# Performance work log

Measured on AMD Instinct MI355X. Metric: run time of the kernel, lower is better.

The kernel has to match this reference:

```python
import jax, jax.numpy as jnp
import numpy as np
import math

N_HEADS = 8
INPUT_DIM = 128
EMBED_DIM = 128
KEY_DIM = EMBED_DIM // N_HEADS  # 16, val_dim == key_dim
BATCH = 4
GRAPH = 2048


def setup_inputs() -> dict:
    key = jax.random.key(0)
    k1, k2, k3, k4, k5 = jax.random.split(key, 5)
    h = jax.random.normal(k1, (BATCH, GRAPH, INPUT_DIM), dtype=jnp.float32)
    # torch.rand -> uniform [0,1)
    W_query = jax.random.uniform(k2, (N_HEADS, INPUT_DIM, KEY_DIM), dtype=jnp.float32)
    W_key = jax.random.uniform(k3, (N_HEADS, INPUT_DIM, KEY_DIM), dtype=jnp.float32)
    W_val = jax.random.uniform(k4, (N_HEADS, INPUT_DIM, KEY_DIM), dtype=jnp.float32)
    W_out = jax.random.uniform(k5, (N_HEADS, KEY_DIM, EMBED_DIM), dtype=jnp.float32)
    return {"h": h, "W_query": W_query, "W_key": W_key, "W_val": W_val, "W_out": W_out}


def reference(h, W_query, W_key, W_val, W_out):
    # q defaults to h (self-attention)
    norm = 1.0 / math.sqrt(KEY_DIM)
    # per-head projections: [H, B, N, dk]
    Q = jnp.einsum('bnd,hdk->hbnk', h, W_query)
    K = jnp.einsum('bnd,hdk->hbnk', h, W_key)
    V = jnp.einsum('bnd,hdv->hbnv', h, W_val)
    compat = norm * jnp.einsum('hbqk,hbnk->hbqn', Q, K)  # [H, B, Nq, N]
    attn = jax.nn.softmax(compat, axis=-1)
    heads = jnp.einsum('hbqn,hbnv->hbqv', attn, V)  # [H, B, Nq, dv]
    out = jnp.einsum('hbqv,hve->bqe', heads, W_out)  # [B, Nq, E]
    return out
```

## Files before the change

### kernel.cpp

```cpp
#include <hip/hip_runtime.h>

typedef __attribute__((ext_vector_type(4))) float f32x4;
typedef __attribute__((ext_vector_type(8))) short bf16x8;

constexpr int NH = 8, D = 128, DK = 16, B = 4, N = 2048;
constexpr int KTILE = 128;
constexpr int NTILES = N / KTILE;
constexpr int TILE_SHORTS = 6144;
constexpr float QSCALE = 0.36067376022224085f;

__device__ __forceinline__ unsigned short f2bf(float f) {
    union { float f; unsigned u; } v; v.f = f;
    return (unsigned short)((v.u + 0x7fffu + ((v.u >> 16) & 1u)) >> 16);
}
__device__ __forceinline__ float bf2f(unsigned short h) {
    union { unsigned u; float f; } v; v.u = ((unsigned)h) << 16; return v.f;
}
__device__ __forceinline__ unsigned pack2(float a, float b) {
    union { float f; unsigned u; } x, y; x.f = a; y.f = b;
    return (x.u >> 16) | (y.u & 0xFFFF0000u);
}
__device__ __forceinline__ float fexp2(float x) {
    float r; asm("v_exp_f32 %0, %1" : "=v"(r) : "v"(x)); return r;
}
__device__ __forceinline__ float fmax3(float a, float b, float c) {
    float r; asm("v_max3_f32 %0, %1, %2, %3" : "=v"(r) : "v"(a), "v"(b), "v"(c));
    return r;
}

__global__ __launch_bounds__(256) void wprep_kernel(
    const float* __restrict__ Wq, const float* __restrict__ Wk,
    const float* __restrict__ Wv, const float* __restrict__ Wo,
    unsigned short* __restrict__ Wf, unsigned short* __restrict__ Wof)
{
    const int t = blockIdx.x * 256 + threadIdx.x;
    if (t < 49152) {
        const int p = t >> 14, r = t & 16383;
        const int head = r >> 11, d = (r >> 4) & 127, kk = r & 15;
        const float wv = (p == 0 ? Wq : p == 1 ? Wk : Wv)[r];
        const unsigned short hi = f2bf(wv);
        const unsigned short lo = f2bf(wv - bf2f(hi));
        const int c = p * 8 + head, s = d >> 4, dd = d & 15;
        const int ch = dd >> 3, j = dd & 7;
        Wf[((c * 8 + s) * 64 + kk + 16 * ch) * 8 + j] = hi;
        Wf[((c * 8 + s) * 64 + kk + 16 * (2 + ch)) * 8 + j] = lo;
    } else {
        const int r = t - 49152;
        const int head = r >> 11, v = (r >> 7) & 15, e = r & 127;
        const float wv = Wo[r];
        const unsigned short hi = f2bf(wv);
        const unsigned short lo = f2bf(wv - bf2f(hi));
        const int c = e >> 4, s = head, ch = v >> 3, j = v & 7;
        Wof[((c * 8 + s) * 64 + (e & 15) + 16 * ch) * 8 + j] = hi;
        Wof[((c * 8 + s) * 64 + (e & 15) + 16 * (2 + ch)) * 8 + j] = lo;
    }
}

constexpr int GR = 32;
__global__ __launch_bounds__(256) void qkv_gemm(
    const float* __restrict__ h, const unsigned short* __restrict__ Wf,
    float* __restrict__ Q, unsigned short* __restrict__ KV)
{
    const int cg6 = blockIdx.x % 6;
    const int cg = cg6 >> 1;
    const int hg = cg6 & 1;
    const int row0 = (blockIdx.x / 6) * GR;
    const int b = row0 >> 11, n0 = row0 & (N - 1);
    const int t = threadIdx.x, w = t >> 6, l = t & 63;
    __shared__ unsigned short hf[8][2][64][8];
    __shared__ unsigned short wfl[4][8][64][8];

    {
        const unsigned short* wsrc = Wf + ((size_t)cg * 8 + hg * 4) * 4096;
        unsigned short* wdst = (unsigned short*)wfl;
        #pragma unroll
        for (int i = 0; i < 8; ++i) {
            const int idx = (t + i * 256) * 8;
            *(uint4*)&wdst[idx] = *(const uint4*)&wsrc[idx];
        }
    }
    #pragma unroll
    for (int pass = 0; pass < 4; ++pass) {
        const int rb = pass * 8 + (t >> 5);
        const int d0 = (t & 31) * 4;
        float4 hv = *(const float4*)&h[(size_t)(row0 + rb) * D + d0];
        const int s = d0 >> 4, ch = (d0 & 15) >> 3, j0 = d0 & 7;
        ushort4 hiv, lov;
        unsigned short* hp = (unsigned short*)&hiv;
        unsigned short* lp = (unsigned short*)&lov;
        #pragma unroll
        for (int i = 0; i < 4; ++i) {
            const float x = ((const float*)&hv)[i];
            const unsigned short hi = f2bf(x);
            hp[i] = hi;
            lp[i] = f2bf(x - bf2f(hi));
        }
        *(ushort4*)&hf[s][rb >> 4][(rb & 15) + 16 * ch][j0] = hiv;
        *(ushort4*)&hf[s][rb >> 4][(rb & 15) + 16 * (2 + ch)][j0] = lov;
    }
    __syncthreads();

    f32x4 acc[2];
    #pragma unroll
    for (int i = 0; i < 2; ++i) acc[i] = (f32x4){0.f, 0.f, 0.f, 0.f};

    for (int s = 0; s < 8; ++s) {
        bf16x8 b1 = *(const bf16x8*)&hf[s][w & 1][l][0];
        bf16x8 b2 = *(const bf16x8*)&hf[s][w & 1][l ^ 32][0];
        #pragma unroll
        for (int ct = 0; ct < 2; ++ct) {
            const int c4 = (w >> 1) * 2 + ct;
            bf16x8 af = *(const bf16x8*)&wfl[c4][s][l][0];
            acc[ct] = __builtin_amdgcn_mfma_f32_16x16x32_bf16(af, b1, acc[ct], 0, 0, 0);
            acc[ct] = __builtin_amdgcn_mfma_f32_16x16x32_bf16(af, b2, acc[ct], 0, 0, 0);
        }
    }

    const int n = n0 + (w & 1) * 16 + (l & 15);
    const int rl = n & 127;
    const int kk0 = (l >> 4) * 4;
    #pragma unroll
    for (int ct = 0; ct < 2; ++ct) {
        const int head = hg * 4 + (w >> 1) * 2 + ct;
        const int hb = head * B + b;
        if (cg == 0) {
            float4 o;
            o.x = acc[ct][0]; o.y = acc[ct][1]; o.z = acc[ct][2]; o.w = acc[ct][3];
            *(float4*)&Q[((size_t)hb * N + n) * DK + kk0] = o;
        } else {
            unsigned short* tb = KV + (size_t)hb * NTILES * TILE_SHORTS
                               + (size_t)(n >> 7) * TILE_SHORTS;
            if (cg == 1) {
                const int gs = kk0 >> 3, j0 = kk0 & 7;
                const int kb2 = rl >> 5, kap = rl & 31;
                const int sub = 2 * kb2 + ((kap >> 2) & 1);
                const int row16 = 4 * (kap >> 3) + (kap & 3);
                ushort4 sh, sl;
                unsigned short* shp = (unsigned short*)&sh;
                unsigned short* slp = (unsigned short*)&sl;
                #pragma unroll
                for (int r = 0; r < 4; ++r) {
                    const unsigned short hi = f2bf(acc[ct][r]);
                    shp[r] = hi;
                    slp[r] = f2bf(acc[ct][r] - bf2f(hi));
                }
                *(ushort4*)&tb[sub * 512 + (row16 + 16 * gs) * 8 + j0] = sh;
                *(ushort4*)&tb[sub * 512 + (row16 + 16 * (2 + gs)) * 8 + j0] = sl;
            } else {
                #pragma unroll
                for (int r = 0; r < 4; ++r) {
                    const int kk = kk0 + r;
                    tb[4096 + kk * 128 + ((rl >> 3) ^ (kk & 7)) * 8 + (rl & 7)]
                        = f2bf(acc[ct][r]);
                }
            }
        }
    }
}

__global__ __launch_bounds__(512, 4) void attn_kernel(
    const float* __restrict__ Q, const unsigned short* __restrict__ KV,
    float* __restrict__ Hd)
{
    const int bid = blockIdx.x;
    const int inner = bid >> 3;
    const int hb = (bid & 7) * 4 + (inner >> 4);
    const int qt = inner & 15;
    const int t = threadIdx.x, w = t >> 6, l = t & 63;
    const int q16 = l & 15, g = l >> 4;
    const size_t qbase = (size_t)hb * N * DK;
    const char* kvb = (const char*)(KV + (size_t)hb * NTILES * TILE_SHORTS);

    __shared__ unsigned short smem[2][TILE_SHORTS];

    const int qrow = qt * 128 + w * 16 + q16;
    bf16x8 qhi, qlo;
    {
        const float* qp = Q + qbase + (size_t)qrow * DK + (g & 1) * 8;
        float4 qa = *(const float4*)qp, qb = *(const float4*)(qp + 4);
        #pragma unroll
        for (int i = 0; i < 8; ++i) {
            const float x = (i < 4 ? ((const float*)&qa)[i] : ((const float*)&qb)[i - 4]) * QSCALE;
            const unsigned short hi = f2bf(x);
            qhi[i] = (short)hi;
            qlo[i] = (short)f2bf(x - bf2f(hi));
        }
    }
    const bf16x8 qf1 = (g < 2) ? qhi : qlo;
    const bf16x8 qf2 = (g < 2) ? qlo : qhi;

    union { unsigned u[4]; bf16x8 v; } ones;
    #pragma unroll
    for (int i = 0; i < 4; ++i) ones.u[i] = 0x3F803F80u;

    f32x4 oacc = {0.f, 0.f, 0.f, 0.f};
    f32x4 lacc = {0.f, 0.f, 0.f, 0.f};
    float m = 0.0f;

    uint4 s0 = *(const uint4*)(kvb + t * 16);
    uint4 s1;
    if (t < 256) s1 = *(const uint4*)(kvb + 8192 + t * 16);
    *(uint4*)((char*)&smem[0][0] + t * 16) = s0;
    if (t < 256) *(uint4*)((char*)&smem[0][0] + 8192 + t * 16) = s1;

    int cur = 0;
    for (int tile = 0; tile < NTILES; ++tile) {
        __syncthreads();
        if (tile + 1 < NTILES) {
            const char* gt = kvb + (size_t)(tile + 1) * 12288;
            s0 = *(const uint4*)(gt + t * 16);
            if (t < 256) s1 = *(const uint4*)(gt + 8192 + t * 16);
        }
        const char* buf = (const char*)&smem[cur][0];

        f32x4 aA[4], aB[4];
        const f32x4 minit = {-m, -m, -m, -m};
        __builtin_amdgcn_s_setprio(1);
        #pragma unroll
        for (int kb = 0; kb < 4; ++kb) {
            bf16x8 kA = *(const bf16x8*)(buf + (2 * kb) * 1024 + l * 16);
            bf16x8 kB = *(const bf16x8*)(buf + (2 * kb + 1) * 1024 + l * 16);
            aA[kb] = __builtin_amdgcn_mfma_f32_16x16x32_bf16(kA, qf1, minit, 0, 0, 0);
            aA[kb] = __builtin_amdgcn_mfma_f32_16x16x32_bf16(kA, qf2, aA[kb], 0, 0, 0);
            aB[kb] = __builtin_amdgcn_mfma_f32_16x16x32_bf16(kB, qf1, minit, 0, 0, 0);
            aB[kb] = __builtin_amdgcn_mfma_f32_16x16x32_bf16(kB, qf2, aB[kb], 0, 0, 0);
        }
        __builtin_amdgcn_s_setprio(0);

        float tm = -3.0e38f;
        #pragma unroll
        for (int kb = 0; kb < 4; ++kb) {
            tm = fmax3(fmax3(aA[kb][0], aA[kb][1], aA[kb][2]),
                       fmax3(aA[kb][3], aB[kb][0], aB[kb][1]),
                       fmax3(aB[kb][2], aB[kb][3], tm));
        }
        if (tile == 0 || !__all(tm <= -30.0f)) {
            if (tile == 0) {
                float d = fmaxf(tm, __shfl_xor(tm, 16));
                d = fmaxf(d, __shfl_xor(d, 32));
                m = d;
                #pragma unroll
                for (int kb = 0; kb < 4; ++kb) {
                    #pragma unroll
                    for (int i = 0; i < 4; ++i) { aA[kb][i] -= d; aB[kb][i] -= d; }
                }
            } else if (!__all(tm <= 8.0f)) {
                float d = fmaxf(tm, __shfl_xor(tm, 16));
                d = fmaxf(d, __shfl_xor(d, 32));
                const float dd = fmaxf(d, 0.f);
                const float sc = fexp2(-dd);
                m += dd;
                oacc *= sc;
                lacc *= sc;
                #pragma unroll
                for (int kb = 0; kb < 4; ++kb) {
                    #pragma unroll
                    for (int i = 0; i < 4; ++i) { aA[kb][i] -= dd; aB[kb][i] -= dd; }
                }
            }
            #pragma unroll
            for (int kb = 0; kb < 4; ++kb) {
                #pragma unroll
                for (int i = 0; i < 4; ++i) {
                    aA[kb][i] = fexp2(aA[kb][i]);
                    aB[kb][i] = fexp2(aB[kb][i]);
                }
            }
            __builtin_amdgcn_s_setprio(1);
            #pragma unroll
            for (int kb = 0; kb < 4; ++kb) {
                union { unsigned u[4]; bf16x8 v; } pf;
                pf.u[0] = pack2(aA[kb][0], aA[kb][1]);
                pf.u[1] = pack2(aA[kb][2], aA[kb][3]);
                pf.u[2] = pack2(aB[kb][0], aB[kb][1]);
                pf.u[3] = pack2(aB[kb][2], aB[kb][3]);
                bf16x8 vf = *(const bf16x8*)(buf + 8192 + q16 * 256 + (((kb * 4 + g) ^ (q16 & 7)) * 16));
                oacc = __builtin_amdgcn_mfma_f32_16x16x32_bf16(vf, pf.v, oacc, 0, 0, 0);
                lacc = __builtin_amdgcn_mfma_f32_16x16x32_bf16(ones.v, pf.v, lacc, 0, 0, 0);
            }
            __builtin_amdgcn_s_setprio(0);
        }

        if (tile + 1 < NTILES) {
            char* nb = (char*)&smem[cur ^ 1][0];
            *(uint4*)(nb + t * 16) = s0;
            if (t < 256) *(uint4*)(nb + 8192 + t * 16) = s1;
        }
        cur ^= 1;
    }

    const float invl = 1.f / lacc[0];
    float4 o;
    o.x = oacc[0] * invl; o.y = oacc[1] * invl;
    o.z = oacc[2] * invl; o.w = oacc[3] * invl;
    *(float4*)(Hd + qbase + (size_t)qrow * DK + g * 4) = o;
}

constexpr int OGR = 16;
__global__ __launch_bounds__(256) void out_gemm(
    const float* __restrict__ Hd, const unsigned short* __restrict__ Wof,
    float* __restrict__ out)
{
    const int row0 = blockIdx.x * OGR;
    const int b = row0 >> 11, n0 = row0 & (N - 1);
    const int t = threadIdx.x, w = t >> 6, l = t & 63;
    __shared__ unsigned short hf[8][64][8];

    #pragma unroll
    for (int pass = 0; pass < 2; ++pass) {
        const int rb = pass * 8 + (t >> 5);
        const int d0 = (t & 31) * 4;
        float4 hv = *(const float4*)&Hd[((size_t)((d0 >> 4) * B + b) * N + (n0 + rb)) * DK + (d0 & 15)];
        const int s = d0 >> 4, ch = (d0 & 15) >> 3, j0 = d0 & 7;
        ushort4 hiv, lov;
        unsigned short* hp = (unsigned short*)&hiv;
        unsigned short* lp = (unsigned short*)&lov;
        #pragma unroll
        for (int i = 0; i < 4; ++i) {
            const float x = ((const float*)&hv)[i];
            const unsigned short hi = f2bf(x);
            hp[i] = hi;
            lp[i] = f2bf(x - bf2f(hi));
        }
        *(ushort4*)&hf[s][rb + 16 * ch][j0] = hiv;
        *(ushort4*)&hf[s][rb + 16 * (2 + ch)][j0] = lov;
    }
    __syncthreads();

    f32x4 acc[2];
    #pragma unroll
    for (int i = 0; i < 2; ++i) acc[i] = (f32x4){0.f, 0.f, 0.f, 0.f};

    bf16x8 afc[2], afn[2];
    #pragma unroll
    for (int ct = 0; ct < 2; ++ct)
        afc[ct] = *(const bf16x8*)&Wof[(((w * 2 + ct) * 8 + 0) * 64 + l) * 8];

    for (int s = 0; s < 8; ++s) {
        if (s + 1 < 8) {
            #pragma unroll
            for (int ct = 0; ct < 2; ++ct)
                afn[ct] = *(const bf16x8*)&Wof[(((w * 2 + ct) * 8 + (s + 1)) * 64 + l) * 8];
        }
        bf16x8 b1 = *(const bf16x8*)&hf[s][l][0];
        bf16x8 b2 = *(const bf16x8*)&hf[s][l ^ 32][0];
        #pragma unroll
        for (int ct = 0; ct < 2; ++ct) {
            acc[ct] = __builtin_amdgcn_mfma_f32_16x16x32_bf16(afc[ct], b1, acc[ct], 0, 0, 0);
            acc[ct] = __builtin_amdgcn_mfma_f32_16x16x32_bf16(afc[ct], b2, acc[ct], 0, 0, 0);
        }
        #pragma unroll
        for (int ct = 0; ct < 2; ++ct) afc[ct] = afn[ct];
    }

    const int n = row0 + (l & 15);
    #pragma unroll
    for (int ct = 0; ct < 2; ++ct) {
        const int c = w * 2 + ct;
        float4 o;
        o.x = acc[ct][0]; o.y = acc[ct][1]; o.z = acc[ct][2]; o.w = acc[ct][3];
        *(float4*)&out[(size_t)n * D + c * 16 + (l >> 4) * 4] = o;
    }
}

extern "C" void kernel_launch(void* const* d_in, const int* in_sizes, int n_in,
                              void* d_out, int out_size, void* d_ws, size_t ws_size,
                              hipStream_t stream) {
    const float* h  = (const float*)d_in[0];
    const float* Wq = (const float*)d_in[1];
    const float* Wk = (const float*)d_in[2];
    const float* Wv = (const float*)d_in[3];
    const float* Wo = (const float*)d_in[4];
    float* out = (float*)d_out;

    char* ws = (char*)d_ws;
    float* Q = (float*)ws;
    unsigned short* KV  = (unsigned short*)(ws + (size_t)4 * 1024 * 1024);
    unsigned short* Wf  = (unsigned short*)(ws + (size_t)10 * 1024 * 1024);
    unsigned short* Wof = (unsigned short*)(ws + (size_t)10 * 1024 * 1024 + 196608);

    wprep_kernel<<<256, 256, 0, stream>>>(Wq, Wk, Wv, Wo, Wf, Wof);
    qkv_gemm<<<(B * N / GR) * 6, 256, 0, stream>>>(h, Wf, Q, KV);
    attn_kernel<<<NH * B * 16, 512, 0, stream>>>(Q, KV, Q);
    out_gemm<<<B * N / OGR, 256, 0, stream>>>(Q, Wof, out);
}
```

Baseline: 54.66 us.

## Split out_gemm columns across two blocks and stage W_out slice in LDS

The output projection grid is doubled so each block computes half of the 128 output columns, with one column tile per wave instead of two. Each block first copies its 32 KB half of the preprocessed W_out into shared memory with coalesced 16-byte loads, then reads the MFMA A-fragments from LDS rather than prefetching them from global memory. This is meant to add parallelism and shorten the per-wave dependency chain in a small tail kernel. The cost is that every row of the attention output is loaded and split into bf16 hi/lo parts twice, and the larger shared-memory footprint may reduce occupancy.

```diff
diff --git a/kernel.cpp b/kernel.cpp
--- a/kernel.cpp
+++ b/kernel.cpp
@@ -301,11 +301,22 @@
     const float* __restrict__ Hd, const unsigned short* __restrict__ Wof,
     float* __restrict__ out)
 {
-    const int row0 = blockIdx.x * OGR;
+    const int cg2 = blockIdx.x & 1;
+    const int row0 = (blockIdx.x >> 1) * OGR;
     const int b = row0 >> 11, n0 = row0 & (N - 1);
     const int t = threadIdx.x, w = t >> 6, l = t & 63;
     __shared__ unsigned short hf[8][64][8];
-
+    __shared__ unsigned short wfl[4][8][64][8];
+
+    {
+        const unsigned short* wsrc = Wof + (size_t)cg2 * 16384;
+        unsigned short* wdst = (unsigned short*)wfl;
+        #pragma unroll
+        for (int i = 0; i < 8; ++i) {
+            const int idx = (t + i * 256) * 8;
+            *(uint4*)&wdst[idx] = *(const uint4*)&wsrc[idx];
+        }
+    }
     #pragma unroll
     for (int pass = 0; pass < 2; ++pass) {
         const int rb = pass * 8 + (t >> 5);
@@ -327,40 +338,20 @@
     }
     __syncthreads();
 
-    f32x4 acc[2];
-    #pragma unroll
-    for (int i = 0; i < 2; ++i) acc[i] = (f32x4){0.f, 0.f, 0.f, 0.f};
-
-    bf16x8 afc[2], afn[2];
-    #pragma unroll
-    for (int ct = 0; ct < 2; ++ct)
-        afc[ct] = *(const bf16x8*)&Wof[(((w * 2 + ct) * 8 + 0) * 64 + l) * 8];
-
+    f32x4 acc = {0.f, 0.f, 0.f, 0.f};
     for (int s = 0; s < 8; ++s) {
-        if (s + 1 < 8) {
-            #pragma unroll
-            for (int ct = 0; ct < 2; ++ct)
-                afn[ct] = *(const bf16x8*)&Wof[(((w * 2 + ct) * 8 + (s + 1)) * 64 + l) * 8];
-        }
         bf16x8 b1 = *(const bf16x8*)&hf[s][l][0];
         bf16x8 b2 = *(const bf16x8*)&hf[s][l ^ 32][0];
-        #pragma unroll
-        for (int ct = 0; ct < 2; ++ct) {
-            acc[ct] = __builtin_amdgcn_mfma_f32_16x16x32_bf16(afc[ct], b1, acc[ct], 0, 0, 0);
-            acc[ct] = __builtin_amdgcn_mfma_f32_16x16x32_bf16(afc[ct], b2, acc[ct], 0, 0, 0);
-        }
-        #pragma unroll
-        for (int ct = 0; ct < 2; ++ct) afc[ct] = afn[ct];
+        bf16x8 af = *(const bf16x8*)&wfl[w][s][l][0];
+        acc = __builtin_amdgcn_mfma_f32_16x16x32_bf16(af, b1, acc, 0, 0, 0);
+        acc = __builtin_amdgcn_mfma_f32_16x16x32_bf16(af, b2, acc, 0, 0, 0);
     }
 
     const int n = row0 + (l & 15);
-    #pragma unroll
-    for (int ct = 0; ct < 2; ++ct) {
-        const int c = w * 2 + ct;
-        float4 o;
-        o.x = acc[ct][0]; o.y = acc[ct][1]; o.z = acc[ct][2]; o.w = acc[ct][3];
-        *(float4*)&out[(size_t)n * D + c * 16 + (l >> 4) * 4] = o;
-    }
+    const int c = cg2 * 4 + w;
+    float4 o;
+    o.x = acc[0]; o.y = acc[1]; o.z = acc[2]; o.w = acc[3];
+    *(float4*)&out[(size_t)n * D + c * 16 + (l >> 4) * 4] = o;
 }
 
 extern "C" void kernel_launch(void* const* d_in, const int* in_sizes, int n_in,
@@ -382,5 +373,5 @@
     wprep_kernel<<<256, 256, 0, stream>>>(Wq, Wk, Wv, Wo, Wf, Wof);
     qkv_gemm<<<(B * N / GR) * 6, 256, 0, stream>>>(h, Wf, Q, KV);
     attn_kernel<<<NH * B * 16, 512, 0, stream>>>(Q, KV, Q);
-    out_gemm<<<B * N / OGR, 256, 0, stream>>>(Q, Wof, out);
-}
+    out_gemm<<<(B * N / OGR) * 2, 256, 0, stream>>>(Q, Wof, out);
+}
```

Result: no change. 55.45 us (+1.4%).
